# Kernel tuning notes

Hardware: AMD Instinct MI355X
Metric: run time of the kernel (lower is better)

The kernel has to match this reference:

```python
import jax, jax.numpy as jnp
import numpy as np

N = 150_000   # total nodes in batched graph
E = 900_000   # total edges (avg in-degree ~ 2*n_gram = 6)
D = 300       # hidden_size_node (GloVe 300d)
B = 512       # number of graphs (docs) in batch
C = 20        # class_num
SLOPE = 0.01  # torch LeakyReLU default negative_slope


def _lrelu(x):
    return jnp.where(x >= 0, x, SLOPE * x)


def setup_inputs() -> dict:
    key = jax.random.key(0)
    ks = jax.random.split(key, 8)
    node_h = jax.random.normal(ks[0], (N, D), dtype=jnp.float32)
    eta = jax.random.uniform(ks[1], (N, 1), dtype=jnp.float32)
    W_attn = jax.random.normal(ks[2], (2 * D, 1), dtype=jnp.float32) * 0.05
    b_attn = jnp.zeros((1,), dtype=jnp.float32)
    W_lin = jax.random.normal(ks[3], (D, C), dtype=jnp.float32) * 0.05
    b_lin = jnp.zeros((C,), dtype=jnp.float32)
    src = jax.random.randint(ks[4], (E,), 0, N, dtype=jnp.int32)
    dst = jax.random.randint(ks[5], (E,), 0, N, dtype=jnp.int32)
    graph_ids = jnp.sort(jax.random.randint(ks[6], (N,), 0, B, dtype=jnp.int32))
    return {
        "node_h": node_h, "eta": eta,
        "W_attn": W_attn, "b_attn": b_attn,
        "W_lin": W_lin, "b_lin": b_lin,
        "src": src, "dst": dst,
        "graph_ids": graph_ids, "num_graphs": B,
    }


def reference(node_h, eta, W_attn, b_attn, W_lin, b_lin, src, dst, graph_ids, num_graphs):
    n = node_h.shape[0]
    # edge_attention: leaky_relu(attn_fc(cat(h_src, h_dst))).
    # cat@W == h_src@W[:D] + h_dst@W[D:], so project per-node first (avoids [E,2D] cat).
    ps = node_h @ W_attn[:D]          # [N,1]
    pd = node_h @ W_attn[D:]          # [N,1]
    w = _lrelu(ps[src] + pd[dst] + b_attn)   # [E,1] edge scores

    # segment softmax over each destination node's mailbox
    deg = jax.ops.segment_sum(jnp.ones((w.shape[0], 1), w.dtype), dst, num_segments=n)  # [N,1]
    wmax = jax.ops.segment_max(w, dst, num_segments=n)
    wmax = jnp.where(deg > 0, wmax, 0.0)     # neutralize -inf for isolated nodes
    ew = jnp.exp(w - wmax[dst])              # [E,1]
    denom = jax.ops.segment_sum(ew, dst, num_segments=n)
    a = ew / jnp.where(denom[dst] > 0, denom[dst], 1.0)   # [E,1] softmax weights

    # gcn_reduce: max over weighted messages a * h_src per destination
    am = a * node_h[src]                      # [E,D]
    agg = jax.ops.segment_max(am, dst, num_segments=n)    # [N,D]
    agg = jnp.where(deg > 0, agg, 0.0)

    # gated update: eta*h + (1-eta)*agg; DGL leaves message-less nodes untouched
    h_new = eta * node_h + (1.0 - eta) * agg
    h_new = jnp.where(deg > 0, h_new, node_h)

    # dgl.sum_nodes per graph, dropout (eval: identity), leaky_relu, classifier
    hg = jax.ops.segment_sum(h_new, graph_ids, num_segments=num_graphs)  # [B,D]
    return _lrelu(hg) @ W_lin + b_lin        # [B,C]
```

## Files before the change

kernel.cpp:

```cpp
#include <hip/hip_runtime.h>
#include <math.h>


#define SLOPE 0.01f
#define KNODES 8

__device__ __forceinline__ float lrelu(float x) { return x >= 0.f ? x : SLOPE * x; }

__device__ __forceinline__ float wrsum(float v) {
#pragma unroll
    for (int m = 32; m >= 1; m >>= 1) v += __shfl_xor(v, m, 64);
    return v;
}
__device__ __forceinline__ float wrmax(float v) {
#pragma unroll
    for (int m = 32; m >= 1; m >>= 1) v = fmaxf(v, __shfl_xor(v, m, 64));
    return v;
}

__global__ __launch_bounds__(256) void k_ps_pd(
    const float* __restrict__ H, const float* __restrict__ Wa,
    float* __restrict__ ps, float* __restrict__ pd, int N, int D) {
    int wid  = (blockIdx.x * blockDim.x + threadIdx.x) >> 6;
    int lane = threadIdx.x & 63;
    if (wid >= N) return;
    const float4* row = (const float4*)(H + (size_t)wid * D);
    const float4* wa0 = (const float4*)Wa;
    const float4* wa1 = (const float4*)(Wa + D);
    int nv = D >> 2;
    float s0 = 0.f, s1 = 0.f;
    for (int v = lane; v < nv; v += 64) {
        float4 h = row[v], a = wa0[v], b = wa1[v];
        s0 += h.x * a.x + h.y * a.y + h.z * a.z + h.w * a.w;
        s1 += h.x * b.x + h.y * b.y + h.z * b.z + h.w * b.w;
    }
    s0 = wrsum(s0);
    s1 = wrsum(s1);
    if (lane == 0) { ps[wid] = s0; pd[wid] = s1; }
}

__global__ __launch_bounds__(256) void k_hist(
    const int* __restrict__ dst, unsigned* __restrict__ deg, int E) {
    int e = blockIdx.x * blockDim.x + threadIdx.x;
    if (e < E) atomicAdd(&deg[dst[e]], 1u);
}

__global__ __launch_bounds__(256) void k_scan1(
    const unsigned* __restrict__ deg, unsigned* __restrict__ offs,
    unsigned* __restrict__ bsum, int N) {
    __shared__ unsigned wsum[4];
    int t = threadIdx.x, b = blockIdx.x;
    int base = b * 1024 + t * 4;
    unsigned v[4];
#pragma unroll
    for (int j = 0; j < 4; j++) { int i = base + j; v[j] = (i < N) ? deg[i] : 0u; }
    unsigned p0 = v[0], p1 = p0 + v[1], p2 = p1 + v[2], p3 = p2 + v[3];
    unsigned tot = p3;
    unsigned x = tot;
    int lane = t & 63, w = t >> 6;
#pragma unroll
    for (int d = 1; d < 64; d <<= 1) { unsigned y = __shfl_up(x, d, 64); if (lane >= d) x += y; }
    if (lane == 63) wsum[w] = x;
    __syncthreads();
    unsigned woff = 0;
    for (int i = 0; i < w; i++) woff += wsum[i];
    unsigned excl = woff + x - tot;
    unsigned incl[4] = {excl + p0, excl + p1, excl + p2, excl + p3};
#pragma unroll
    for (int j = 0; j < 4; j++) { int i = base + j; if (i < N) offs[i + 1] = incl[j]; }
    if (t == 255) bsum[b] = excl + tot;
}

__global__ __launch_bounds__(256) void k_scan2(
    const unsigned* __restrict__ bsum, unsigned* __restrict__ bpre, int nT) {
    __shared__ unsigned wsum[4];
    int t = threadIdx.x;
    unsigned v[8], p[8];
    unsigned run = 0;
#pragma unroll
    for (int j = 0; j < 8; j++) { int i = t * 8 + j; v[j] = (i < nT) ? bsum[i] : 0u; run += v[j]; p[j] = run; }
    unsigned tot = run, x = tot;
    int lane = t & 63, w = t >> 6;
#pragma unroll
    for (int d = 1; d < 64; d <<= 1) { unsigned y = __shfl_up(x, d, 64); if (lane >= d) x += y; }
    if (lane == 63) wsum[w] = x;
    __syncthreads();
    unsigned woff = 0;
    for (int i = 0; i < w; i++) woff += wsum[i];
    unsigned excl = woff + x - tot;
#pragma unroll
    for (int j = 0; j < 8; j++) { int i = t * 8 + j; if (i < nT) bpre[i] = excl + (j ? p[j - 1] : 0u); }
}

__global__ __launch_bounds__(256) void k_scan3(
    unsigned* __restrict__ offs, const unsigned* __restrict__ bpre, int N) {
    int i = blockIdx.x * blockDim.x + threadIdx.x;
    if (i == 0) offs[0] = 0u;
    if (i < N) offs[i + 1] += bpre[i >> 10];
}

__global__ __launch_bounds__(256) void k_scatter(
    const int* __restrict__ src, const int* __restrict__ dst,
    const unsigned* __restrict__ offs, unsigned* __restrict__ cur,
    int* __restrict__ ssrc, int E) {
    int e = blockIdx.x * blockDim.x + threadIdx.x;
    if (e >= E) return;
    int d = dst[e];
    unsigned r = atomicAdd(&cur[d], 1u);
    ssrc[offs[d] + r] = src[e];
}

__global__ __launch_bounds__(256) void k_fused(
    const float* __restrict__ H, const float* __restrict__ eta,
    const float* __restrict__ ps, const float* __restrict__ pd,
    const float* __restrict__ battn,
    const unsigned* __restrict__ offs, const int* __restrict__ ssrc,
    const int* __restrict__ gid, float* __restrict__ hg,
    int N, int D) {
    int wid  = (blockIdx.x * blockDim.x + threadIdx.x) >> 6;
    int lane = threadIdx.x & 63;
    int n0 = wid * KNODES;
    if (n0 >= N) return;
    int n1 = min(n0 + KNODES, N);
    int nv = D >> 2;
    bool q0 = lane < nv;
    bool q1 = (64 + lane) < nv;
    float b0 = battn[0];

    float sx = 0.f, sy = 0.f, sz = 0.f, sw = 0.f;
    float tx = 0.f, ty = 0.f, tz = 0.f, tw = 0.f;
    int curg = gid[n0];

    for (int n = n0; n < n1; ++n) {
        unsigned e0 = offs[n], e1 = offs[n + 1];
        int degn = (int)(e1 - e0);
        const float4* hrow = (const float4*)(H + (size_t)n * D);
        float4 h0 = {0, 0, 0, 0}, h1 = {0, 0, 0, 0};
        if (q0) h0 = hrow[lane];
        if (q1) h1 = hrow[64 + lane];
        float hx = h0.x, hy = h0.y, hz = h0.z, hw = h0.w;
        float gx = h1.x, gy = h1.y, gz = h1.z, gw = h1.w;
        if (degn > 0) {
            float pdn = pd[n] + b0;
            float ax = -INFINITY, ay = -INFINITY, az = -INFINITY, aw = -INFINITY;
            float bx = -INFINITY, by = -INFINITY, bz = -INFINITY, bw = -INFINITY;
            if (degn <= 64) {
                int   sn_l = (lane < degn) ? ssrc[e0 + lane] : 0;
                float w_l  = (lane < degn) ? lrelu(ps[sn_l] + pdn) : -INFINITY;
                float m    = wrmax(w_l);
                float ex   = (lane < degn) ? expf(w_l - m) : 0.f;
                float s    = wrsum(ex);
                float a_l  = ex * (1.f / s);
                int e = 0;
                for (; e + 1 < degn; e += 2) {
                    float a0s = __shfl(a_l, e, 64);
                    int   sn0 = __shfl(sn_l, e, 64);
                    float a1s = __shfl(a_l, e + 1, 64);
                    int   sn1 = __shfl(sn_l, e + 1, 64);
                    const float4* r0 = (const float4*)(H + (size_t)sn0 * D);
                    const float4* r1 = (const float4*)(H + (size_t)sn1 * D);
                    if (q0) {
                        float4 u = r0[lane];
                        float4 v = r1[lane];
                        ax = fmaxf(fmaxf(ax, a0s * u.x), a1s * v.x);
                        ay = fmaxf(fmaxf(ay, a0s * u.y), a1s * v.y);
                        az = fmaxf(fmaxf(az, a0s * u.z), a1s * v.z);
                        aw = fmaxf(fmaxf(aw, a0s * u.w), a1s * v.w);
                    }
                    if (q1) {
                        float4 u = r0[64 + lane];
                        float4 v = r1[64 + lane];
                        bx = fmaxf(fmaxf(bx, a0s * u.x), a1s * v.x);
                        by = fmaxf(fmaxf(by, a0s * u.y), a1s * v.y);
                        bz = fmaxf(fmaxf(bz, a0s * u.z), a1s * v.z);
                        bw = fmaxf(fmaxf(bw, a0s * u.w), a1s * v.w);
                    }
                }
                if (e < degn) {
                    float a  = __shfl(a_l, e, 64);
                    int   sn = __shfl(sn_l, e, 64);
                    const float4* srow = (const float4*)(H + (size_t)sn * D);
                    if (q0) {
                        float4 v0 = srow[lane];
                        ax = fmaxf(ax, a * v0.x); ay = fmaxf(ay, a * v0.y);
                        az = fmaxf(az, a * v0.z); aw = fmaxf(aw, a * v0.w);
                    }
                    if (q1) {
                        float4 v1 = srow[64 + lane];
                        bx = fmaxf(bx, a * v1.x); by = fmaxf(by, a * v1.y);
                        bz = fmaxf(bz, a * v1.z); bw = fmaxf(bw, a * v1.w);
                    }
                }
            } else {
                float mm = -INFINITY;
                for (unsigned e = e0 + lane; e < e1; e += 64)
                    mm = fmaxf(mm, lrelu(ps[ssrc[e]] + pdn));
                float m = wrmax(mm);
                float ssum = 0.f;
                for (unsigned e = e0 + lane; e < e1; e += 64)
                    ssum += expf(lrelu(ps[ssrc[e]] + pdn) - m);
                float s = wrsum(ssum), inv = 1.f / s;
                for (unsigned e = e0; e < e1; ++e) {
                    int sn = ssrc[e];
                    float a = expf(lrelu(ps[sn] + pdn) - m) * inv;
                    const float4* srow = (const float4*)(H + (size_t)sn * D);
                    if (q0) {
                        float4 v0 = srow[lane];
                        ax = fmaxf(ax, a * v0.x); ay = fmaxf(ay, a * v0.y);
                        az = fmaxf(az, a * v0.z); aw = fmaxf(aw, a * v0.w);
                    }
                    if (q1) {
                        float4 v1 = srow[64 + lane];
                        bx = fmaxf(bx, a * v1.x); by = fmaxf(by, a * v1.y);
                        bz = fmaxf(bz, a * v1.z); bw = fmaxf(bw, a * v1.w);
                    }
                }
            }
            float et = eta[n], om = 1.f - et;
            hx = et * h0.x + om * ax; hy = et * h0.y + om * ay;
            hz = et * h0.z + om * az; hw = et * h0.w + om * aw;
            gx = et * h1.x + om * bx; gy = et * h1.y + om * by;
            gz = et * h1.z + om * bz; gw = et * h1.w + om * bw;
        }
        int g = gid[n];
        if (g != curg) {
            float* row = hg + (size_t)curg * D;
            int c = 4 * lane;
            if (q0) {
                atomicAdd(&row[c + 0], sx); atomicAdd(&row[c + 1], sy);
                atomicAdd(&row[c + 2], sz); atomicAdd(&row[c + 3], sw);
            }
            if (q1) {
                int c1 = 4 * (64 + lane);
                atomicAdd(&row[c1 + 0], tx); atomicAdd(&row[c1 + 1], ty);
                atomicAdd(&row[c1 + 2], tz); atomicAdd(&row[c1 + 3], tw);
            }
            sx = sy = sz = sw = tx = ty = tz = tw = 0.f;
            curg = g;
        }
        sx += hx; sy += hy; sz += hz; sw += hw;
        if (q1) { tx += gx; ty += gy; tz += gz; tw += gw; }
    }
    float* row = hg + (size_t)curg * D;
    int c = 4 * lane;
    if (q0) {
        atomicAdd(&row[c + 0], sx); atomicAdd(&row[c + 1], sy);
        atomicAdd(&row[c + 2], sz); atomicAdd(&row[c + 3], sw);
    }
    if (q1) {
        int c1 = 4 * (64 + lane);
        atomicAdd(&row[c1 + 0], tx); atomicAdd(&row[c1 + 1], ty);
        atomicAdd(&row[c1 + 2], tz); atomicAdd(&row[c1 + 3], tw);
    }
}

__global__ __launch_bounds__(64) void k_out(
    const float* __restrict__ hg, const float* __restrict__ Wl,
    const float* __restrict__ bl, float* __restrict__ out,
    int D, int C) {
    int b = blockIdx.x;
    int c = threadIdx.x;
    if (c >= C) return;
    const float* row = hg + (size_t)b * D;
    float acc = 0.f;
    for (int d = 0; d < D; ++d)
        acc += lrelu(row[d]) * Wl[(size_t)d * C + c];
    out[(size_t)b * C + c] = acc + bl[c];
}

extern "C" void kernel_launch(void* const* d_in, const int* in_sizes, int n_in,
                              void* d_out, int out_size, void* d_ws, size_t ws_size,
                              hipStream_t stream) {
    const float* H   = (const float*)d_in[0];
    const float* eta = (const float*)d_in[1];
    const float* Wa  = (const float*)d_in[2];
    const float* ba  = (const float*)d_in[3];
    const float* Wl  = (const float*)d_in[4];
    const float* bl  = (const float*)d_in[5];
    const int*   src = (const int*)d_in[6];
    const int*   dst = (const int*)d_in[7];
    const int*   gid = (const int*)d_in[8];

    const int N = in_sizes[1];
    const int D = in_sizes[2] / 2;
    const int C = in_sizes[5];
    const int E = in_sizes[6];
    const int B = out_size / C;

    char* w = (char*)d_ws;
    float*    ps   = (float*)w;    w += (size_t)N * 4;
    float*    pd   = (float*)w;    w += (size_t)N * 4;
    unsigned* deg  = (unsigned*)w; w += (size_t)N * 4;
    unsigned* cur  = (unsigned*)w; w += (size_t)N * 4;
    float*    hg   = (float*)w;    w += (size_t)B * D * 4;
    unsigned* offs = (unsigned*)w; w += (size_t)(N + 1) * 4;
    unsigned* bsum = (unsigned*)w; w += 2048 * 4;
    unsigned* bpre = (unsigned*)w; w += 2048 * 4;
    int*      ssrc = (int*)w;      w += (size_t)E * 4;

    hipMemsetAsync(deg, 0, (size_t)(2 * N + (size_t)B * D) * 4, stream);

    const int nT = (N + 1023) / 1024;

    k_ps_pd<<<dim3((N + 3) / 4), dim3(256), 0, stream>>>(H, Wa, ps, pd, N, D);
    k_hist<<<dim3((E + 255) / 256), dim3(256), 0, stream>>>(dst, deg, E);
    k_scan1<<<dim3(nT), dim3(256), 0, stream>>>(deg, offs, bsum, N);
    k_scan2<<<dim3(1), dim3(256), 0, stream>>>(bsum, bpre, nT);
    k_scan3<<<dim3((N + 255) / 256), dim3(256), 0, stream>>>(offs, bpre, N);
    k_scatter<<<dim3((E + 255) / 256), dim3(256), 0, stream>>>(src, dst, offs, cur, ssrc, E);
    {
        int waves  = (N + KNODES - 1) / KNODES;
        int blocks = (waves + 3) / 4;
        k_fused<<<dim3(blocks), dim3(256), 0, stream>>>(H, eta, ps, pd, ba, offs, ssrc, gid, hg, N, D);
    }
    k_out<<<dim3(B), dim3(64), 0, stream>>>(hg, Wl, bl, (float*)d_out, D, C);
}
```

Before: 674.2 us.

## Merge prep kernels, fold scan stages into consumers, unroll gather by four

Merges the ps/pd projection, the degree histogram and the zeroing of cur/hg into one launch, replacing most of the memset. The second and third scan stages are dropped: each consumer block recomputes the block prefix from bsum into shared memory and adds it to local offsets. The aggregation loop is unrolled to four source rows per step so more gathers are in flight. This cuts launch count and one pass over the offsets, at the cost of a redundant small prefix scan and an extra __syncthreads in every block of scatter and fused.

```diff
diff --git a/kernel.cpp b/kernel.cpp
--- a/kernel.cpp
+++ b/kernel.cpp
@@ -4,6 +4,7 @@
 
 #define SLOPE 0.01f
 #define KNODES 8
+#define MAXT 192
 
 __device__ __forceinline__ float lrelu(float x) { return x >= 0.f ? x : SLOPE * x; }
 
@@ -18,35 +19,65 @@
     return v;
 }
 
-__global__ __launch_bounds__(256) void k_ps_pd(
+__device__ __forceinline__ void compute_bpre(const unsigned* __restrict__ bsum,
+                                             int nT, unsigned* lb) {
+    if (threadIdx.x < 64) {
+        int l = threadIdx.x;
+        unsigned a0 = (3 * l     < nT) ? bsum[3 * l]     : 0u;
+        unsigned a1 = (3 * l + 1 < nT) ? bsum[3 * l + 1] : 0u;
+        unsigned a2 = (3 * l + 2 < nT) ? bsum[3 * l + 2] : 0u;
+        unsigned tot = a0 + a1 + a2, x = tot;
+#pragma unroll
+        for (int d = 1; d < 64; d <<= 1) {
+            unsigned y = __shfl_up(x, d, 64);
+            if (l >= d) x += y;
+        }
+        unsigned excl = x - tot;
+        if (3 * l     < nT) lb[3 * l]     = excl;
+        if (3 * l + 1 < nT) lb[3 * l + 1] = excl + a0;
+        if (3 * l + 2 < nT) lb[3 * l + 2] = excl + a0 + a1;
+    }
+    __syncthreads();
+}
+
+__global__ __launch_bounds__(256) void k_prep(
     const float* __restrict__ H, const float* __restrict__ Wa,
-    float* __restrict__ ps, float* __restrict__ pd, int N, int D) {
-    int wid  = (blockIdx.x * blockDim.x + threadIdx.x) >> 6;
-    int lane = threadIdx.x & 63;
-    if (wid >= N) return;
-    const float4* row = (const float4*)(H + (size_t)wid * D);
-    const float4* wa0 = (const float4*)Wa;
-    const float4* wa1 = (const float4*)(Wa + D);
-    int nv = D >> 2;
-    float s0 = 0.f, s1 = 0.f;
-    for (int v = lane; v < nv; v += 64) {
-        float4 h = row[v], a = wa0[v], b = wa1[v];
-        s0 += h.x * a.x + h.y * a.y + h.z * a.z + h.w * a.w;
-        s1 += h.x * b.x + h.y * b.y + h.z * b.z + h.w * b.w;
-    }
-    s0 = wrsum(s0);
-    s1 = wrsum(s1);
-    if (lane == 0) { ps[wid] = s0; pd[wid] = s1; }
-}
-
-__global__ __launch_bounds__(256) void k_hist(
-    const int* __restrict__ dst, unsigned* __restrict__ deg, int E) {
-    int e = blockIdx.x * blockDim.x + threadIdx.x;
-    if (e < E) atomicAdd(&deg[dst[e]], 1u);
+    const int* __restrict__ dst,
+    float* __restrict__ ps, float* __restrict__ pd,
+    unsigned* __restrict__ deg,
+    unsigned* __restrict__ zbase, size_t zn,
+    int N, int D, int E, int nb_ps, int nb_hist) {
+    int b = blockIdx.x;
+    if (b < nb_ps) {
+        int wid  = b * 4 + (threadIdx.x >> 6);
+        int lane = threadIdx.x & 63;
+        if (wid >= N) return;
+        const float4* row = (const float4*)(H + (size_t)wid * D);
+        const float4* wa0 = (const float4*)Wa;
+        const float4* wa1 = (const float4*)(Wa + D);
+        int nv = D >> 2;
+        float s0 = 0.f, s1 = 0.f;
+        for (int v = lane; v < nv; v += 64) {
+            float4 h = row[v], a = wa0[v], c = wa1[v];
+            s0 += h.x * a.x + h.y * a.y + h.z * a.z + h.w * a.w;
+            s1 += h.x * c.x + h.y * c.y + h.z * c.z + h.w * c.w;
+        }
+        s0 = wrsum(s0);
+        s1 = wrsum(s1);
+        if (lane == 0) { ps[wid] = s0; pd[wid] = s1; }
+    } else if (b < nb_ps + nb_hist) {
+        int e = (b - nb_ps) * 256 + threadIdx.x;
+        if (e < E) atomicAdd(&deg[dst[e]], 1u);
+    } else {
+        int    nbz    = gridDim.x - nb_ps - nb_hist;
+        size_t i      = (size_t)(b - nb_ps - nb_hist) * 256 + threadIdx.x;
+        size_t stride = (size_t)nbz * 256;
+        for (; i < zn; i += stride) zbase[i] = 0u;
+    }
 }
 
 __global__ __launch_bounds__(256) void k_scan1(
-    const unsigned* __restrict__ deg, unsigned* __restrict__ offs,
+    const unsigned* __restrict__ deg, unsigned* __restrict__ loffs,
     unsigned* __restrict__ bsum, int N) {
     __shared__ unsigned wsum[4];
     int t = threadIdx.x, b = blockIdx.x;
@@ -54,8 +85,8 @@
     unsigned v[4];
 #pragma unroll
     for (int j = 0; j < 4; j++) { int i = base + j; v[j] = (i < N) ? deg[i] : 0u; }
-    unsigned p0 = v[0], p1 = p0 + v[1], p2 = p1 + v[2], p3 = p2 + v[3];
-    unsigned tot = p3;
+    unsigned p0 = v[0], p1 = p0 + v[1], p2 = p1 + v[2];
+    unsigned tot = p2 + v[3];
     unsigned x = tot;
     int lane = t & 63, w = t >> 6;
 #pragma unroll
@@ -65,58 +96,36 @@
     unsigned woff = 0;
     for (int i = 0; i < w; i++) woff += wsum[i];
     unsigned excl = woff + x - tot;
-    unsigned incl[4] = {excl + p0, excl + p1, excl + p2, excl + p3};
-#pragma unroll
-    for (int j = 0; j < 4; j++) { int i = base + j; if (i < N) offs[i + 1] = incl[j]; }
+    unsigned o[4] = {excl, excl + p0, excl + p1, excl + p2};
+#pragma unroll
+    for (int j = 0; j < 4; j++) { int i = base + j; if (i < N) loffs[i] = o[j]; }
     if (t == 255) bsum[b] = excl + tot;
-}
-
-__global__ __launch_bounds__(256) void k_scan2(
-    const unsigned* __restrict__ bsum, unsigned* __restrict__ bpre, int nT) {
-    __shared__ unsigned wsum[4];
-    int t = threadIdx.x;
-    unsigned v[8], p[8];
-    unsigned run = 0;
-#pragma unroll
-    for (int j = 0; j < 8; j++) { int i = t * 8 + j; v[j] = (i < nT) ? bsum[i] : 0u; run += v[j]; p[j] = run; }
-    unsigned tot = run, x = tot;
-    int lane = t & 63, w = t >> 6;
-#pragma unroll
-    for (int d = 1; d < 64; d <<= 1) { unsigned y = __shfl_up(x, d, 64); if (lane >= d) x += y; }
-    if (lane == 63) wsum[w] = x;
-    __syncthreads();
-    unsigned woff = 0;
-    for (int i = 0; i < w; i++) woff += wsum[i];
-    unsigned excl = woff + x - tot;
-#pragma unroll
-    for (int j = 0; j < 8; j++) { int i = t * 8 + j; if (i < nT) bpre[i] = excl + (j ? p[j - 1] : 0u); }
-}
-
-__global__ __launch_bounds__(256) void k_scan3(
-    unsigned* __restrict__ offs, const unsigned* __restrict__ bpre, int N) {
-    int i = blockIdx.x * blockDim.x + threadIdx.x;
-    if (i == 0) offs[0] = 0u;
-    if (i < N) offs[i + 1] += bpre[i >> 10];
 }
 
 __global__ __launch_bounds__(256) void k_scatter(
     const int* __restrict__ src, const int* __restrict__ dst,
-    const unsigned* __restrict__ offs, unsigned* __restrict__ cur,
-    int* __restrict__ ssrc, int E) {
-    int e = blockIdx.x * blockDim.x + threadIdx.x;
+    const unsigned* __restrict__ loffs, const unsigned* __restrict__ bsum,
+    unsigned* __restrict__ cur, int* __restrict__ ssrc, int E, int nT) {
+    __shared__ unsigned lb[MAXT];
+    compute_bpre(bsum, nT, lb);
+    int e = blockIdx.x * 256 + threadIdx.x;
     if (e >= E) return;
     int d = dst[e];
+    unsigned base = loffs[d] + lb[d >> 10];
     unsigned r = atomicAdd(&cur[d], 1u);
-    ssrc[offs[d] + r] = src[e];
+    ssrc[base + r] = src[e];
 }
 
 __global__ __launch_bounds__(256) void k_fused(
     const float* __restrict__ H, const float* __restrict__ eta,
     const float* __restrict__ ps, const float* __restrict__ pd,
     const float* __restrict__ battn,
-    const unsigned* __restrict__ offs, const int* __restrict__ ssrc,
-    const int* __restrict__ gid, float* __restrict__ hg,
-    int N, int D) {
+    const unsigned* __restrict__ loffs, const unsigned* __restrict__ bsum,
+    const int* __restrict__ ssrc, const int* __restrict__ gid,
+    float* __restrict__ hg, int N, int D, int E, int nT) {
+    __shared__ unsigned lb[MAXT];
+    compute_bpre(bsum, nT, lb);
+
     int wid  = (blockIdx.x * blockDim.x + threadIdx.x) >> 6;
     int lane = threadIdx.x & 63;
     int n0 = wid * KNODES;
@@ -132,7 +141,8 @@
     int curg = gid[n0];
 
     for (int n = n0; n < n1; ++n) {
-        unsigned e0 = offs[n], e1 = offs[n + 1];
+        unsigned e0 = loffs[n] + lb[n >> 10];
+        unsigned e1 = (n + 1 < N) ? (loffs[n + 1] + lb[(n + 1) >> 10]) : (unsigned)E;
         int degn = (int)(e1 - e0);
         const float4* hrow = (const float4*)(H + (size_t)n * D);
         float4 h0 = {0, 0, 0, 0}, h1 = {0, 0, 0, 0};
@@ -152,28 +162,48 @@
                 float s    = wrsum(ex);
                 float a_l  = ex * (1.f / s);
                 int e = 0;
+                for (; e + 3 < degn; e += 4) {
+                    float a0s = __shfl(a_l, e, 64),     a1s = __shfl(a_l, e + 1, 64);
+                    float a2s = __shfl(a_l, e + 2, 64), a3s = __shfl(a_l, e + 3, 64);
+                    int   s0i = __shfl(sn_l, e, 64),     s1i = __shfl(sn_l, e + 1, 64);
+                    int   s2i = __shfl(sn_l, e + 2, 64), s3i = __shfl(sn_l, e + 3, 64);
+                    const float4* r0 = (const float4*)(H + (size_t)s0i * D);
+                    const float4* r1 = (const float4*)(H + (size_t)s1i * D);
+                    const float4* r2 = (const float4*)(H + (size_t)s2i * D);
+                    const float4* r3 = (const float4*)(H + (size_t)s3i * D);
+                    if (q0) {
+                        float4 u0 = r0[lane], u1 = r1[lane], u2 = r2[lane], u3 = r3[lane];
+                        ax = fmaxf(fmaxf(fmaxf(ax, a0s * u0.x), a1s * u1.x), fmaxf(a2s * u2.x, a3s * u3.x));
+                        ay = fmaxf(fmaxf(fmaxf(ay, a0s * u0.y), a1s * u1.y), fmaxf(a2s * u2.y, a3s * u3.y));
+                        az = fmaxf(fmaxf(fmaxf(az, a0s * u0.z), a1s * u1.z), fmaxf(a2s * u2.z, a3s * u3.z));
+                        aw = fmaxf(fmaxf(fmaxf(aw, a0s * u0.w), a1s * u1.w), fmaxf(a2s * u2.w, a3s * u3.w));
+                    }
+                    if (q1) {
+                        float4 u0 = r0[64 + lane], u1 = r1[64 + lane], u2 = r2[64 + lane], u3 = r3[64 + lane];
+                        bx = fmaxf(fmaxf(fmaxf(bx, a0s * u0.x), a1s * u1.x), fmaxf(a2s * u2.x, a3s * u3.x));
+                        by = fmaxf(fmaxf(fmaxf(by, a0s * u0.y), a1s * u1.y), fmaxf(a2s * u2.y, a3s * u3.y));
+                        bz = fmaxf(fmaxf(fmaxf(bz, a0s * u0.z), a1s * u1.z), fmaxf(a2s * u2.z, a3s * u3.z));
+                        bw = fmaxf(fmaxf(fmaxf(bw, a0s * u0.w), a1s * u1.w), fmaxf(a2s * u2.w, a3s * u3.w));
+                    }
+                }
                 for (; e + 1 < degn; e += 2) {
-                    float a0s = __shfl(a_l, e, 64);
-                    int   sn0 = __shfl(sn_l, e, 64);
-                    float a1s = __shfl(a_l, e + 1, 64);
-                    int   sn1 = __shfl(sn_l, e + 1, 64);
-                    const float4* r0 = (const float4*)(H + (size_t)sn0 * D);
-                    const float4* r1 = (const float4*)(H + (size_t)sn1 * D);
+                    float a0s = __shfl(a_l, e, 64), a1s = __shfl(a_l, e + 1, 64);
+                    int   s0i = __shfl(sn_l, e, 64), s1i = __shfl(sn_l, e + 1, 64);
+                    const float4* r0 = (const float4*)(H + (size_t)s0i * D);
+                    const float4* r1 = (const float4*)(H + (size_t)s1i * D);
                     if (q0) {
-                        float4 u = r0[lane];
-                        float4 v = r1[lane];
-                        ax = fmaxf(fmaxf(ax, a0s * u.x), a1s * v.x);
-                        ay = fmaxf(fmaxf(ay, a0s * u.y), a1s * v.y);
-                        az = fmaxf(fmaxf(az, a0s * u.z), a1s * v.z);
-                        aw = fmaxf(fmaxf(aw, a0s * u.w), a1s * v.w);
+                        float4 u0 = r0[lane], u1 = r1[lane];
+                        ax = fmaxf(fmaxf(ax, a0s * u0.x), a1s * u1.x);
+                        ay = fmaxf(fmaxf(ay, a0s * u0.y), a1s * u1.y);
+                        az = fmaxf(fmaxf(az, a0s * u0.z), a1s * u1.z);
+                        aw = fmaxf(fmaxf(aw, a0s * u0.w), a1s * u1.w);
                     }
                     if (q1) {
-                        float4 u = r0[64 + lane];
-                        float4 v = r1[64 + lane];
-                        bx = fmaxf(fmaxf(bx, a0s * u.x), a1s * v.x);
-                        by = fmaxf(fmaxf(by, a0s * u.y), a1s * v.y);
-                        bz = fmaxf(fmaxf(bz, a0s * u.z), a1s * v.z);
-                        bw = fmaxf(fmaxf(bw, a0s * u.w), a1s * v.w);
+                        float4 u0 = r0[64 + lane], u1 = r1[64 + lane];
+                        bx = fmaxf(fmaxf(bx, a0s * u0.x), a1s * u1.x);
+                        by = fmaxf(fmaxf(by, a0s * u0.y), a1s * u1.y);
+                        bz = fmaxf(fmaxf(bz, a0s * u0.z), a1s * u1.z);
+                        bw = fmaxf(fmaxf(bw, a0s * u0.w), a1s * u1.w);
                     }
                 }
                 if (e < degn) {
@@ -288,30 +318,33 @@
     const int B = out_size / C;
 
     char* w = (char*)d_ws;
-    float*    ps   = (float*)w;    w += (size_t)N * 4;
-    float*    pd   = (float*)w;    w += (size_t)N * 4;
-    unsigned* deg  = (unsigned*)w; w += (size_t)N * 4;
-    unsigned* cur  = (unsigned*)w; w += (size_t)N * 4;
-    float*    hg   = (float*)w;    w += (size_t)B * D * 4;
-    unsigned* offs = (unsigned*)w; w += (size_t)(N + 1) * 4;
-    unsigned* bsum = (unsigned*)w; w += 2048 * 4;
-    unsigned* bpre = (unsigned*)w; w += 2048 * 4;
-    int*      ssrc = (int*)w;      w += (size_t)E * 4;
-
-    hipMemsetAsync(deg, 0, (size_t)(2 * N + (size_t)B * D) * 4, stream);
-
-    const int nT = (N + 1023) / 1024;
-
-    k_ps_pd<<<dim3((N + 3) / 4), dim3(256), 0, stream>>>(H, Wa, ps, pd, N, D);
-    k_hist<<<dim3((E + 255) / 256), dim3(256), 0, stream>>>(dst, deg, E);
-    k_scan1<<<dim3(nT), dim3(256), 0, stream>>>(deg, offs, bsum, N);
-    k_scan2<<<dim3(1), dim3(256), 0, stream>>>(bsum, bpre, nT);
-    k_scan3<<<dim3((N + 255) / 256), dim3(256), 0, stream>>>(offs, bpre, N);
-    k_scatter<<<dim3((E + 255) / 256), dim3(256), 0, stream>>>(src, dst, offs, cur, ssrc, E);
+    float*    ps    = (float*)w;    w += (size_t)N * 4;
+    float*    pd    = (float*)w;    w += (size_t)N * 4;
+    unsigned* deg   = (unsigned*)w; w += (size_t)N * 4;
+    unsigned* cur   = (unsigned*)w; w += (size_t)N * 4;
+    float*    hg    = (float*)w;    w += (size_t)B * D * 4;
+    unsigned* loffs = (unsigned*)w; w += (size_t)N * 4;
+    unsigned* bsum  = (unsigned*)w; w += 256 * 4;
+    int*      ssrc  = (int*)w;      w += (size_t)E * 4;
+
+    hipMemsetAsync(deg, 0, (size_t)N * 4, stream);
+
+    const int nT      = (N + 1023) / 1024;
+    const int nb_ps   = (N + 3) / 4;
+    const int nb_hist = (E + 255) / 256;
+    const int nb_zero = 256;
+    const size_t zn   = (size_t)N + (size_t)B * D;
+
+    k_prep<<<dim3(nb_ps + nb_hist + nb_zero), dim3(256), 0, stream>>>(
+        H, Wa, dst, ps, pd, deg, cur, zn, N, D, E, nb_ps, nb_hist);
+    k_scan1<<<dim3(nT), dim3(256), 0, stream>>>(deg, loffs, bsum, N);
+    k_scatter<<<dim3((E + 255) / 256), dim3(256), 0, stream>>>(
+        src, dst, loffs, bsum, cur, ssrc, E, nT);
     {
         int waves  = (N + KNODES - 1) / KNODES;
         int blocks = (waves + 3) / 4;
-        k_fused<<<dim3(blocks), dim3(256), 0, stream>>>(H, eta, ps, pd, ba, offs, ssrc, gid, hg, N, D);
+        k_fused<<<dim3(blocks), dim3(256), 0, stream>>>(
+            H, eta, ps, pd, ba, loffs, bsum, ssrc, gid, hg, N, D, E, nT);
     }
     k_out<<<dim3(B), dim3(64), 0, stream>>>(hg, Wl, bl, (float*)d_out, D, C);
 }
```

Result: slower. 688.1 us (+2.1%).
